# Kernel tuning notes

Measured on AMD Instinct MI355X. Metric: run time of the kernel, lower is better.

The kernel has to match this reference:

```python
import jax, jax.numpy as jnp
import numpy as np

N_NODES = 100000
N_EDGES = 1600000
IN_DIM = 128
HID = 128
OUT_DIM = 64
N_LAYERS = 3


def setup_inputs() -> dict:
    key = jax.random.key(0)
    ks = jax.random.split(key, 8)
    x = jax.random.normal(ks[0], (N_NODES, IN_DIM), dtype=jnp.float32)
    edge_index = jax.random.randint(ks[1], (2, N_EDGES), 0, N_NODES, dtype=jnp.int64)
    s = 1.0 / np.sqrt(HID)
    Wl = jax.random.normal(ks[2], (N_LAYERS, HID, HID), dtype=jnp.float32) * s
    Wr = jax.random.normal(ks[3], (N_LAYERS, HID, HID), dtype=jnp.float32) * s
    b = jnp.zeros((N_LAYERS, HID), dtype=jnp.float32)
    fc_w = jax.random.normal(ks[4], (N_LAYERS * HID, OUT_DIM), dtype=jnp.float32) * (1.0 / np.sqrt(N_LAYERS * HID))
    fc_b = jnp.zeros((OUT_DIM,), dtype=jnp.float32)
    return {"x": x, "edge_index": edge_index, "Wl": Wl, "Wr": Wr, "b": b, "fc_w": fc_w, "fc_b": fc_b}


def _sage_conv(x, src, dst, Wl, Wr, b, n_nodes):
    # PyG SAGEConv (aggr='mean'): out = lin_l(mean_{j->i} x_j) + lin_r(x_i)
    msg = x[src]                                             # [E, d] gather
    agg = jax.ops.segment_sum(msg, dst, num_segments=n_nodes)  # [N, d]
    deg = jax.ops.segment_sum(jnp.ones((src.shape[0],), x.dtype), dst, num_segments=n_nodes)
    mean = agg / jnp.maximum(deg, 1.0)[:, None]
    return mean @ Wl + x @ Wr + b


def reference(x, edge_index, Wl, Wr, b, fc_w, fc_b):
    src, dst = edge_index[0], edge_index[1]
    n = x.shape[0]
    h = x
    layer_out = []
    for i in range(N_LAYERS):  # small fixed layer count
        h = jax.nn.relu(_sage_conv(h, src, dst, Wl[i], Wr[i], b[i], n))
        layer_out.append(h)  # dropout p=0 -> identity
    hk = jnp.concatenate(layer_out, axis=-1)  # JK 'cat': [N, L*HID]
    return hk @ fc_w + fc_b
```

## Files before the change

kernel.cpp:

```cpp
#include <hip/hip_runtime.h>
#include <hip/hip_bf16.h>
#include <stdint.h>

#define N_NODES 100000
#define N_EDGES 1600000
#define HID 128
#define OUT_DIM 64
#define N_LAYERS 3
#define CAP 64
#define CAP_SHIFT 6
#define BIN_NODES 256
#define NBIN2 ((N_NODES + BIN_NODES - 1) / BIN_NODES)
#define BINCAP 8192
#define EPT 8
#define P1_BLOCKS ((N_EDGES + 256 * EPT - 1) / (256 * EPT))

typedef __attribute__((ext_vector_type(8))) short short8;
typedef __attribute__((ext_vector_type(4))) float v4f;
typedef __attribute__((ext_vector_type(4))) unsigned short ushort4v;

__device__ __forceinline__ float bf2f(unsigned int lo16) {
    union { unsigned int i; float f; } v; v.i = lo16 << 16; return v.f;
}
__device__ __forceinline__ unsigned short f2bf(float f) {
    union { float f; unsigned int i; } v; v.f = f;
    unsigned int r = v.i + 0x7fffu + ((v.i >> 16) & 1u);
    return (unsigned short)(r >> 16);
}

__device__ __forceinline__ void stage16(const void* g, void* l) {
    __builtin_amdgcn_global_load_lds(
        (const __attribute__((address_space(1))) unsigned int*)g,
        (__attribute__((address_space(3))) unsigned int*)l, 16, 0, 0);
}

#define CONV_N (N_NODES * HID / 4)
__global__ __launch_bounds__(256) void merged_pre(
    const int* __restrict__ raw,
    int* __restrict__ bin_cnt, unsigned int* __restrict__ bins,
    const float* __restrict__ x, unsigned short* __restrict__ xb,
    const float* __restrict__ Wl, const float* __restrict__ Wr,
    const float* __restrict__ fc_w,
    unsigned short* __restrict__ WlT, unsigned short* __restrict__ WrT,
    unsigned short* __restrict__ fcT,
    unsigned short* b0, unsigned short* b1, unsigned short* b2) {
    __shared__ int h[NBIN2];
    __shared__ int basekeep[NBIN2];
    __shared__ int sflag;
    int blk = blockIdx.x, tid = threadIdx.x;

    if (blk < P1_BLOCKS) {
        if (tid < 64) {
            int v = raw[2 * tid + 1];
            unsigned long long bl = __ballot(v != 0);
            if (tid == 0) sflag = (bl == 0ull) ? 1 : 0;
        }
        for (int b = tid; b < NBIN2; b += 256) h[b] = 0;
        __syncthreads();
        bool is64 = (sflag != 0);

        int e0 = blk * (256 * EPT) + tid;
        int s[EPT], d[EPT];
#pragma unroll
        for (int k = 0; k < EPT; ++k) {
            int e = e0 + k * 256;
            if (e < N_EDGES) {
                if (is64) {
                    const long long* r = (const long long*)raw;
                    d[k] = (int)r[N_EDGES + e];
                    s[k] = (int)r[e];
                } else {
                    d[k] = raw[N_EDGES + e];
                    s[k] = raw[e];
                }
            } else {
                d[k] = -1;
            }
        }
#pragma unroll
        for (int k = 0; k < EPT; ++k)
            if (d[k] >= 0) atomicAdd(&h[d[k] >> 8], 1);
        __syncthreads();
        for (int b = tid; b < NBIN2; b += 256) {
            int c = h[b];
            basekeep[b] = c ? atomicAdd(&bin_cnt[b], c) : 0;
            h[b] = 0;
        }
        __syncthreads();
#pragma unroll
        for (int k = 0; k < EPT; ++k) {
            if (d[k] >= 0) {
                int b = d[k] >> 8;
                int off = basekeep[b] + atomicAdd(&h[b], 1);
                if (off < BINCAP)
                    bins[(size_t)b * BINCAP + off] =
                        ((unsigned int)s[k] << 8) | (unsigned int)(d[k] & 255);
            }
        }
    }

    if (blk == P1_BLOCKS && tid < 192) {
        unsigned short* bufs[3] = {b0, b1, b2};
        uint32_t* p = (uint32_t*)bufs[tid >> 6];
        p[(size_t)N_NODES * 64 + (tid & 63)] = 0;
    }

    int gidx = blk * 256 + tid;
    if (gidx < CONV_N) {
        float4 v = ((const float4*)x)[gidx];
        ushort4v o;
        o[0] = f2bf(v.x); o[1] = f2bf(v.y); o[2] = f2bf(v.z); o[3] = f2bf(v.w);
        ((ushort4v*)xb)[gidx] = o;
    } else {
        int idx = gidx - CONV_N;
        const int WELEMS = N_LAYERS * HID * HID;
        if (idx < WELEMS) {
            int l = idx / (HID * HID);
            int rem = idx - l * HID * HID;
            int k = rem / HID, nn2 = rem - k * HID;
            WlT[l * HID * HID + nn2 * HID + k] = f2bf(Wl[idx]);
            WrT[l * HID * HID + nn2 * HID + k] = f2bf(Wr[idx]);
        } else {
            int j = idx - WELEMS;
            if (j < N_LAYERS * HID * OUT_DIM) {
                int l = j / (HID * OUT_DIM);
                int rem = j - l * HID * OUT_DIM;
                int k = rem / OUT_DIM, o = rem - k * OUT_DIM;
                fcT[l * OUT_DIM * HID + o * HID + k] = f2bf(fc_w[(l * HID + k) * OUT_DIM + o]);
            }
        }
    }
}

__global__ __launch_bounds__(256) void fill_p2(const int* __restrict__ bin_cnt,
                                               const unsigned int* __restrict__ bins,
                                               int* __restrict__ ell,
                                               int* __restrict__ deg,
                                               float* __restrict__ inv_deg, int n) {
    __shared__ int tile[BIN_NODES * CAP];
    __shared__ int cnt[BIN_NODES];
    int b = blockIdx.x, tid = threadIdx.x;
    for (int i = tid; i < BIN_NODES; i += 256) cnt[i] = 0;
    __syncthreads();

    int m = bin_cnt[b];
    if (m > BINCAP) m = BINCAP;
    for (int i = tid; i < m; i += 256) {
        unsigned int e = bins[(size_t)b * BINCAP + i];
        int dl = (int)(e & 255u);
        int slot = atomicAdd(&cnt[dl], 1);
        if (slot < CAP) tile[(dl << CAP_SHIFT) + slot] = (int)(e >> 8);
    }
    __syncthreads();

    int node0 = b << 8;
    for (int i = tid; i < BIN_NODES; i += 256) {
        int node = node0 + i;
        if (node < n) {
            int dgf = cnt[i];
            int dg = dgf > CAP ? CAP : dgf;
            deg[node] = dg;
            inv_deg[node] = 1.0f / (float)(dg > 0 ? dg : 1);
            int r = (dg + 7) & ~7;
            for (int p = dg; p < r; ++p) tile[(i << CAP_SHIFT) + p] = N_NODES;
        }
    }
    __syncthreads();

    const uint4* t4 = (const uint4*)tile;
    uint4* g4 = (uint4*)ell;
    for (int v = tid; v < BIN_NODES * 16; v += 256) {
        int row = v >> 4;
        int node = node0 + row;
        if (node < n) g4[((size_t)node << 4) + (v & 15)] = t4[v];
    }
}

__device__ __forceinline__ void gather8(const uint4* __restrict__ hv,
                                        int4 i0, int4 i1, int lane16, uint4 v[8]) {
    v[0] = hv[(size_t)i0.x * 16 + lane16];
    v[1] = hv[(size_t)i0.y * 16 + lane16];
    v[2] = hv[(size_t)i0.z * 16 + lane16];
    v[3] = hv[(size_t)i0.w * 16 + lane16];
    v[4] = hv[(size_t)i1.x * 16 + lane16];
    v[5] = hv[(size_t)i1.y * 16 + lane16];
    v[6] = hv[(size_t)i1.z * 16 + lane16];
    v[7] = hv[(size_t)i1.w * 16 + lane16];
}
__device__ __forceinline__ void accum8(const uint4 v[8], float a[8]) {
#pragma unroll
    for (int u = 0; u < 8; ++u) {
        a[0] += bf2f(v[u].x & 0xffffu); a[1] += bf2f(v[u].x >> 16);
        a[2] += bf2f(v[u].y & 0xffffu); a[3] += bf2f(v[u].y >> 16);
        a[4] += bf2f(v[u].z & 0xffffu); a[5] += bf2f(v[u].z >> 16);
        a[6] += bf2f(v[u].w & 0xffffu); a[7] += bf2f(v[u].w >> 16);
    }
}

__global__ __launch_bounds__(256) void agg_bf(
    const unsigned short* __restrict__ h, const int* __restrict__ ell,
    const int* __restrict__ deg, const float* __restrict__ inv_deg,
    unsigned short* __restrict__ meanb) {
    int tid = threadIdx.x;
    int grp = tid >> 4;
    int lane16 = tid & 15;
    int node = blockIdx.x * 16 + grp;
    bool valid = node < N_NODES;
    int nd = valid ? node : 0;
    int dg = valid ? deg[nd] : 0;
    int dgp = (dg + 7) & ~7;
    int base = nd << CAP_SHIFT;
    const uint4* hv = (const uint4*)h;
    float a[8];
#pragma unroll
    for (int c = 0; c < 8; ++c) a[c] = 0.f;

    if (dgp) {
        uint4 vA[8], vB[8];
        int4 i0 = *(const int4*)&ell[base + 0];
        int4 i1 = *(const int4*)&ell[base + 4];
        gather8(hv, i0, i1, lane16, vA);
        int t = 8;
        bool done = false;
        while (t < dgp) {
            i0 = *(const int4*)&ell[base + t];
            i1 = *(const int4*)&ell[base + t + 4];
            gather8(hv, i0, i1, lane16, vB);
            accum8(vA, a);
            t += 8;
            if (t >= dgp) { accum8(vB, a); done = true; break; }
            i0 = *(const int4*)&ell[base + t];
            i1 = *(const int4*)&ell[base + t + 4];
            gather8(hv, i0, i1, lane16, vA);
            accum8(vB, a);
            t += 8;
        }
        if (!done) accum8(vA, a);
    }
    if (valid) {
        float id = inv_deg[nd];
        uint4 o;
        o.x = (uint32_t)f2bf(a[0] * id) | ((uint32_t)f2bf(a[1] * id) << 16);
        o.y = (uint32_t)f2bf(a[2] * id) | ((uint32_t)f2bf(a[3] * id) << 16);
        o.z = (uint32_t)f2bf(a[4] * id) | ((uint32_t)f2bf(a[5] * id) << 16);
        o.w = (uint32_t)f2bf(a[6] * id) | ((uint32_t)f2bf(a[7] * id) << 16);
        *(uint4*)&meanb[(size_t)node * HID + lane16 * 8] = o;
    }
}

__global__ __launch_bounds__(256, 2) void layer_mfma(
    const unsigned short* __restrict__ Am,
    const unsigned short* __restrict__ Ah,
    const unsigned short* __restrict__ WlT,
    const unsigned short* __restrict__ WrT,
    const float* __restrict__ bias,
    unsigned short* __restrict__ Hout, int n) {
    __shared__ uint4 smA[128 * 16];
    __shared__ uint4 smB[128 * 16];
    int tid = threadIdx.x;
    int w = tid >> 6, L = tid & 63;
    int q = L >> 4, r16 = L & 15;
    int colbase = (w & 1) * 64;
    int nodebase = (w >> 1) * 64;
    int node0 = blockIdx.x * 128;

    {
        const unsigned short* srcs[2] = {Am, Ah};
#pragma unroll
        for (int op = 0; op < 2; ++op) {
            const unsigned short* S = srcs[op];
            char* D = (char*)(op ? smB : smA);
#pragma unroll
            for (int i = 0; i < 8; ++i) {
                int c = (w << 3) + i;
                int row_l = (c << 2) + (L >> 4);
                int chunk = (L & 15) ^ (row_l & 7);
                const unsigned short* src =
                    S + (((size_t)(node0 + row_l)) << 7) + (chunk << 3);
                stage16(src, D + (c << 10));
            }
        }
    }

    short8 wfr[2][4][4];
#pragma unroll
    for (int seg = 0; seg < 2; ++seg) {
        const unsigned short* WT = seg ? WrT : WlT;
#pragma unroll
        for (int t = 0; t < 4; ++t)
#pragma unroll
            for (int i = 0; i < 4; ++i)
                wfr[seg][t][i] =
                    *(const short8*)&WT[(colbase + i * 16 + r16) * HID + t * 32 + q * 8];
    }

    __syncthreads();

    v4f acc[4][4];
#pragma unroll
    for (int i = 0; i < 4; ++i)
#pragma unroll
        for (int j = 0; j < 4; ++j)
#pragma unroll
            for (int r = 0; r < 4; ++r) acc[i][j][r] = 0.f;

#pragma unroll
    for (int seg = 0; seg < 2; ++seg) {
        const uint4* SM = seg ? smB : smA;
#pragma unroll
        for (int t = 0; t < 4; ++t) {
            short8 bfr[4];
#pragma unroll
            for (int j = 0; j < 4; ++j) {
                int row = nodebase + j * 16 + r16;
                bfr[j] = *(const short8*)&SM[(row << 4) + ((t * 4 + q) ^ (row & 7))];
            }
#pragma unroll
            for (int i = 0; i < 4; ++i)
#pragma unroll
                for (int j = 0; j < 4; ++j)
                    acc[i][j] = __builtin_amdgcn_mfma_f32_16x16x32_bf16(
                        wfr[seg][t][i], bfr[j], acc[i][j], 0, 0, 0);
        }
    }

#pragma unroll
    for (int i = 0; i < 4; ++i) {
        int col = colbase + i * 16 + q * 4;
        float4 bv = *(const float4*)&bias[col];
#pragma unroll
        for (int j = 0; j < 4; ++j) {
            int node = node0 + nodebase + j * 16 + r16;
            if (node < n) {
                float v0 = acc[i][j][0] + bv.x;
                float v1 = acc[i][j][1] + bv.y;
                float v2 = acc[i][j][2] + bv.z;
                float v3 = acc[i][j][3] + bv.w;
                ushort4v o;
                o[0] = f2bf(v0 > 0.f ? v0 : 0.f);
                o[1] = f2bf(v1 > 0.f ? v1 : 0.f);
                o[2] = f2bf(v2 > 0.f ? v2 : 0.f);
                o[3] = f2bf(v3 > 0.f ? v3 : 0.f);
                *(ushort4v*)&Hout[(size_t)node * HID + col] = o;
            }
        }
    }
}

__global__ __launch_bounds__(256, 2) void layer3_fc(
    const unsigned short* __restrict__ Am,
    const unsigned short* __restrict__ Ah,
    const unsigned short* __restrict__ WlT,
    const unsigned short* __restrict__ WrT,
    const float* __restrict__ bias,
    const unsigned short* __restrict__ hA,
    const unsigned short* __restrict__ fcT,
    const float* __restrict__ fc_b,
    float* __restrict__ out, int n) {
    __shared__ uint4 smA[128 * 16];
    __shared__ uint4 smB[128 * 16];
    int tid = threadIdx.x;
    int w = tid >> 6, L = tid & 63;
    int q = L >> 4, r16 = L & 15;
    int colbase = (w & 1) * 64;
    int nodebase = (w >> 1) * 64;
    int node0 = blockIdx.x * 128;

    {
        const unsigned short* srcs[2] = {Am, Ah};
#pragma unroll
        for (int op = 0; op < 2; ++op) {
            const unsigned short* S = srcs[op];
            char* D = (char*)(op ? smB : smA);
#pragma unroll
            for (int i = 0; i < 8; ++i) {
                int c = (w << 3) + i;
                int row_l = (c << 2) + (L >> 4);
                int chunk = (L & 15) ^ (row_l & 7);
                const unsigned short* src =
                    S + (((size_t)(node0 + row_l)) << 7) + (chunk << 3);
                stage16(src, D + (c << 10));
            }
        }
    }

    short8 wfr[2][4][4];
#pragma unroll
    for (int seg = 0; seg < 2; ++seg) {
        const unsigned short* WT = seg ? WrT : WlT;
#pragma unroll
        for (int t = 0; t < 4; ++t)
#pragma unroll
            for (int i = 0; i < 4; ++i)
                wfr[seg][t][i] =
                    *(const short8*)&WT[(colbase + i * 16 + r16) * HID + t * 32 + q * 8];
    }

    __syncthreads();

    v4f acc[4][4];
#pragma unroll
    for (int i = 0; i < 4; ++i)
#pragma unroll
        for (int j = 0; j < 4; ++j)
#pragma unroll
            for (int r = 0; r < 4; ++r) acc[i][j][r] = 0.f;

#pragma unroll
    for (int seg = 0; seg < 2; ++seg) {
        const uint4* SM = seg ? smB : smA;
#pragma unroll
        for (int t = 0; t < 4; ++t) {
            short8 bfr[4];
#pragma unroll
            for (int j = 0; j < 4; ++j) {
                int row = nodebase + j * 16 + r16;
                bfr[j] = *(const short8*)&SM[(row << 4) + ((t * 4 + q) ^ (row & 7))];
            }
#pragma unroll
            for (int i = 0; i < 4; ++i)
#pragma unroll
                for (int j = 0; j < 4; ++j)
                    acc[i][j] = __builtin_amdgcn_mfma_f32_16x16x32_bf16(
                        wfr[seg][t][i], bfr[j], acc[i][j], 0, 0, 0);
        }
    }

    int nd2[2], gvalid[2];
#pragma unroll
    for (int j = 0; j < 2; ++j) {
        int t = node0 + w * 32 + j * 16 + r16;
        gvalid[j] = t < n;
        nd2[j] = gvalid[j] ? t : n - 1;
    }
    short8 ha[2][4];
#pragma unroll
    for (int j = 0; j < 2; ++j)
#pragma unroll
        for (int t = 0; t < 4; ++t)
            ha[j][t] = *(const short8*)&hA[(size_t)nd2[j] * HID + t * 32 + q * 8];

    __syncthreads();

#pragma unroll
    for (int i = 0; i < 4; ++i) {
        int col = colbase + i * 16 + q * 4;
        float4 bv = *(const float4*)&bias[col];
#pragma unroll
        for (int j = 0; j < 4; ++j) {
            int row = nodebase + j * 16 + r16;
            float v0 = acc[i][j][0] + bv.x;
            float v1 = acc[i][j][1] + bv.y;
            float v2 = acc[i][j][2] + bv.z;
            float v3 = acc[i][j][3] + bv.w;
            uint2 val;
            val.x = (uint32_t)f2bf(v0 > 0.f ? v0 : 0.f) |
                    ((uint32_t)f2bf(v1 > 0.f ? v1 : 0.f) << 16);
            val.y = (uint32_t)f2bf(v2 > 0.f ? v2 : 0.f) |
                    ((uint32_t)f2bf(v3 > 0.f ? v3 : 0.f) << 16);
            int slot = (col >> 3) ^ (row & 7);
            uint2* p2 = (uint2*)&smA[(row << 4) + slot];
            p2[q & 1] = val;
        }
    }
    __syncthreads();

    v4f acc2[4][2];
#pragma unroll
    for (int i = 0; i < 4; ++i) {
        float4 bv = *(const float4*)&fc_b[i * 16 + q * 4];
#pragma unroll
        for (int j = 0; j < 2; ++j) {
            acc2[i][j][0] = bv.x; acc2[i][j][1] = bv.y;
            acc2[i][j][2] = bv.z; acc2[i][j][3] = bv.w;
        }
    }

#pragma unroll
    for (int l = 0; l < 3; ++l) {
        const unsigned short* F = fcT + (size_t)l * OUT_DIM * HID;
#pragma unroll
        for (int t = 0; t < 4; ++t) {
            int koff = t * 32 + q * 8;
            short8 afr[4], bfr[2];
#pragma unroll
            for (int i = 0; i < 4; ++i)
                afr[i] = *(const short8*)&F[(i * 16 + r16) * HID + koff];
#pragma unroll
            for (int j = 0; j < 2; ++j) {
                int row = w * 32 + j * 16 + r16;
                if (l == 0)
                    bfr[j] = ha[j][t];
                else if (l == 1)
                    bfr[j] = *(const short8*)&smB[(row << 4) + ((t * 4 + q) ^ (row & 7))];
                else
                    bfr[j] = *(const short8*)&smA[(row << 4) + ((t * 4 + q) ^ (row & 7))];
            }
#pragma unroll
            for (int i = 0; i < 4; ++i)
#pragma unroll
                for (int j = 0; j < 2; ++j)
                    acc2[i][j] = __builtin_amdgcn_mfma_f32_16x16x32_bf16(afr[i], bfr[j], acc2[i][j], 0, 0, 0);
        }
    }

#pragma unroll
    for (int i = 0; i < 4; ++i)
#pragma unroll
        for (int j = 0; j < 2; ++j)
            if (gvalid[j])
                *(v4f*)&out[(size_t)nd2[j] * OUT_DIM + i * 16 + q * 4] = acc2[i][j];
}

extern "C" void kernel_launch(void* const* d_in, const int* in_sizes, int n_in,
                              void* d_out, int out_size, void* d_ws, size_t ws_size,
                              hipStream_t stream) {
    const float* x     = (const float*)d_in[0];
    const int*   edges = (const int*)d_in[1];
    const float* Wl    = (const float*)d_in[2];
    const float* Wr    = (const float*)d_in[3];
    const float* b     = (const float*)d_in[4];
    const float* fc_w  = (const float*)d_in[5];
    const float* fc_b  = (const float*)d_in[6];
    float* out = (float*)d_out;

    char* ws = (char*)d_ws;
    size_t off = 0;
    auto alloc = [&](size_t bytes) {
        void* p = ws + off;
        off = (off + bytes + 255) & ~(size_t)255;
        return p;
    };
    int*   bin_cnt = (int*)alloc((size_t)NBIN2 * 4);
    int*   deg     = (int*)alloc((size_t)N_NODES * 4);
    float* inv_deg = (float*)alloc((size_t)N_NODES * 4);
    int*   ell     = (int*)alloc(((size_t)N_NODES * CAP + 64) * 4);
    unsigned int* bins = (unsigned int*)alloc((size_t)NBIN2 * BINCAP * 4);
    unsigned short* xb    = (unsigned short*)alloc((size_t)(N_NODES + 128) * HID * 2);
    unsigned short* meanb = (unsigned short*)alloc((size_t)(N_NODES + 128) * HID * 2);
    unsigned short* hA    = (unsigned short*)alloc((size_t)(N_NODES + 128) * HID * 2);
    unsigned short* hB    = (unsigned short*)alloc((size_t)(N_NODES + 128) * HID * 2);
    unsigned short* WlT   = (unsigned short*)alloc((size_t)N_LAYERS * HID * HID * 2);
    unsigned short* WrT   = (unsigned short*)alloc((size_t)N_LAYERS * HID * HID * 2);
    unsigned short* fcT   = (unsigned short*)alloc((size_t)N_LAYERS * OUT_DIM * HID * 2);

    hipMemsetAsync(bin_cnt, 0, (size_t)NBIN2 * 4, stream);

    const int PREP_TOTAL = CONV_N + N_LAYERS * HID * HID + N_LAYERS * HID * OUT_DIM;
    int pregrid = (PREP_TOTAL + 255) / 256;
    merged_pre<<<pregrid, 256, 0, stream>>>(
        edges, bin_cnt, bins, x, xb, Wl, Wr, fc_w, WlT, WrT, fcT, xb, hA, hB);
    fill_p2<<<NBIN2, 256, 0, stream>>>(bin_cnt, bins, ell, deg, inv_deg, N_NODES);

    int ngrid = (N_NODES + 127) / 128;
    int agrid = (N_NODES + 15) / 16;

    agg_bf<<<agrid, 256, 0, stream>>>(xb, ell, deg, inv_deg, meanb);
    layer_mfma<<<ngrid, 256, 0, stream>>>(
        meanb, xb, WlT, WrT, b, hA, N_NODES);

    agg_bf<<<agrid, 256, 0, stream>>>(hA, ell, deg, inv_deg, meanb);
    layer_mfma<<<ngrid, 256, 0, stream>>>(
        meanb, hA, WlT + (size_t)HID * HID, WrT + (size_t)HID * HID, b + HID, hB, N_NODES);

    agg_bf<<<agrid, 256, 0, stream>>>(hB, ell, deg, inv_deg, meanb);
    layer3_fc<<<ngrid, 256, 0, stream>>>(
        meanb, hB, WlT + (size_t)2 * HID * HID, WrT + (size_t)2 * HID * HID, b + 2 * HID,
        hA, fcT, fc_b, out, N_NODES);
}
```

Before: 446.6 us.

## Simplify aggregation loop and shrink layer GEMM tile to 64 nodes for occupancy

The aggregation kernel drops its manual double-buffered gather pipeline for a simple per-8-neighbor loop with scalar index loads, leaving latency hiding to the compiler and occupancy. The layer GEMM kernel now handles 64 nodes per block, with each wave owning 32 output columns, which halves shared memory and accumulator registers and raises the launch-bounds occupancy hint from 2 to 4. The cost is less in-flight memory parallelism per thread in aggregation and more blocks, with weight fragments reloaded for each smaller tile.

```diff
diff --git a/kernel.cpp b/kernel.cpp
--- a/kernel.cpp
+++ b/kernel.cpp
@@ -176,27 +176,6 @@
     }
 }
 
-__device__ __forceinline__ void gather8(const uint4* __restrict__ hv,
-                                        int4 i0, int4 i1, int lane16, uint4 v[8]) {
-    v[0] = hv[(size_t)i0.x * 16 + lane16];
-    v[1] = hv[(size_t)i0.y * 16 + lane16];
-    v[2] = hv[(size_t)i0.z * 16 + lane16];
-    v[3] = hv[(size_t)i0.w * 16 + lane16];
-    v[4] = hv[(size_t)i1.x * 16 + lane16];
-    v[5] = hv[(size_t)i1.y * 16 + lane16];
-    v[6] = hv[(size_t)i1.z * 16 + lane16];
-    v[7] = hv[(size_t)i1.w * 16 + lane16];
-}
-__device__ __forceinline__ void accum8(const uint4 v[8], float a[8]) {
-#pragma unroll
-    for (int u = 0; u < 8; ++u) {
-        a[0] += bf2f(v[u].x & 0xffffu); a[1] += bf2f(v[u].x >> 16);
-        a[2] += bf2f(v[u].y & 0xffffu); a[3] += bf2f(v[u].y >> 16);
-        a[4] += bf2f(v[u].z & 0xffffu); a[5] += bf2f(v[u].z >> 16);
-        a[6] += bf2f(v[u].w & 0xffffu); a[7] += bf2f(v[u].w >> 16);
-    }
-}
-
 __global__ __launch_bounds__(256) void agg_bf(
     const unsigned short* __restrict__ h, const int* __restrict__ ell,
     const int* __restrict__ deg, const float* __restrict__ inv_deg,
@@ -215,27 +194,20 @@
 #pragma unroll
     for (int c = 0; c < 8; ++c) a[c] = 0.f;
 
-    if (dgp) {
-        uint4 vA[8], vB[8];
-        int4 i0 = *(const int4*)&ell[base + 0];
-        int4 i1 = *(const int4*)&ell[base + 4];
-        gather8(hv, i0, i1, lane16, vA);
-        int t = 8;
-        bool done = false;
-        while (t < dgp) {
-            i0 = *(const int4*)&ell[base + t];
-            i1 = *(const int4*)&ell[base + t + 4];
-            gather8(hv, i0, i1, lane16, vB);
-            accum8(vA, a);
-            t += 8;
-            if (t >= dgp) { accum8(vB, a); done = true; break; }
-            i0 = *(const int4*)&ell[base + t];
-            i1 = *(const int4*)&ell[base + t + 4];
-            gather8(hv, i0, i1, lane16, vA);
-            accum8(vB, a);
-            t += 8;
-        }
-        if (!done) accum8(vA, a);
+    for (int t = 0; t < dgp; t += 8) {
+        int idx[8];
+#pragma unroll
+        for (int u = 0; u < 8; ++u) idx[u] = ell[base + t + u];
+        uint4 v[8];
+#pragma unroll
+        for (int u = 0; u < 8; ++u) v[u] = hv[(size_t)idx[u] * 16 + lane16];
+#pragma unroll
+        for (int u = 0; u < 8; ++u) {
+            a[0] += bf2f(v[u].x & 0xffffu); a[1] += bf2f(v[u].x >> 16);
+            a[2] += bf2f(v[u].y & 0xffffu); a[3] += bf2f(v[u].y >> 16);
+            a[4] += bf2f(v[u].z & 0xffffu); a[5] += bf2f(v[u].z >> 16);
+            a[6] += bf2f(v[u].w & 0xffffu); a[7] += bf2f(v[u].w >> 16);
+        }
     }
     if (valid) {
         float id = inv_deg[nd];
@@ -248,21 +220,20 @@
     }
 }
 
-__global__ __launch_bounds__(256, 2) void layer_mfma(
+__global__ __launch_bounds__(256, 4) void layer_mfma(
     const unsigned short* __restrict__ Am,
     const unsigned short* __restrict__ Ah,
     const unsigned short* __restrict__ WlT,
     const unsigned short* __restrict__ WrT,
     const float* __restrict__ bias,
     unsigned short* __restrict__ Hout, int n) {
-    __shared__ uint4 smA[128 * 16];
-    __shared__ uint4 smB[128 * 16];
+    __shared__ uint4 smA[64 * 16];
+    __shared__ uint4 smB[64 * 16];
     int tid = threadIdx.x;
     int w = tid >> 6, L = tid & 63;
     int q = L >> 4, r16 = L & 15;
-    int colbase = (w & 1) * 64;
-    int nodebase = (w >> 1) * 64;
-    int node0 = blockIdx.x * 128;
+    int colbase = w << 5;
+    int node0 = blockIdx.x * 64;
 
     {
         const unsigned short* srcs[2] = {Am, Ah};
@@ -271,8 +242,8 @@
             const unsigned short* S = srcs[op];
             char* D = (char*)(op ? smB : smA);
 #pragma unroll
-            for (int i = 0; i < 8; ++i) {
-                int c = (w << 3) + i;
+            for (int i = 0; i < 4; ++i) {
+                int c = (w << 2) + i;
                 int row_l = (c << 2) + (L >> 4);
                 int chunk = (L & 15) ^ (row_l & 7);
                 const unsigned short* src =
@@ -282,23 +253,23 @@
         }
     }
 
-    short8 wfr[2][4][4];
+    short8 wfr[2][4][2];
 #pragma unroll
     for (int seg = 0; seg < 2; ++seg) {
         const unsigned short* WT = seg ? WrT : WlT;
 #pragma unroll
         for (int t = 0; t < 4; ++t)
 #pragma unroll
-            for (int i = 0; i < 4; ++i)
+            for (int i = 0; i < 2; ++i)
                 wfr[seg][t][i] =
                     *(const short8*)&WT[(colbase + i * 16 + r16) * HID + t * 32 + q * 8];
     }
 
     __syncthreads();
 
-    v4f acc[4][4];
-#pragma unroll
-    for (int i = 0; i < 4; ++i)
+    v4f acc[2][4];
+#pragma unroll
+    for (int i = 0; i < 2; ++i)
 #pragma unroll
         for (int j = 0; j < 4; ++j)
 #pragma unroll
@@ -312,11 +283,11 @@
             short8 bfr[4];
 #pragma unroll
             for (int j = 0; j < 4; ++j) {
-                int row = nodebase + j * 16 + r16;
+                int row = j * 16 + r16;
                 bfr[j] = *(const short8*)&SM[(row << 4) + ((t * 4 + q) ^ (row & 7))];
             }
 #pragma unroll
-            for (int i = 0; i < 4; ++i)
+            for (int i = 0; i < 2; ++i)
 #pragma unroll
                 for (int j = 0; j < 4; ++j)
                     acc[i][j] = __builtin_amdgcn_mfma_f32_16x16x32_bf16(
@@ -325,12 +296,12 @@
     }
 
 #pragma unroll
-    for (int i = 0; i < 4; ++i) {
+    for (int i = 0; i < 2; ++i) {
         int col = colbase + i * 16 + q * 4;
         float4 bv = *(const float4*)&bias[col];
 #pragma unroll
         for (int j = 0; j < 4; ++j) {
-            int node = node0 + nodebase + j * 16 + r16;
+            int node = node0 + j * 16 + r16;
             if (node < n) {
                 float v0 = acc[i][j][0] + bv.x;
                 float v1 = acc[i][j][1] + bv.y;
@@ -552,19 +523,20 @@
         edges, bin_cnt, bins, x, xb, Wl, Wr, fc_w, WlT, WrT, fcT, xb, hA, hB);
     fill_p2<<<NBIN2, 256, 0, stream>>>(bin_cnt, bins, ell, deg, inv_deg, N_NODES);
 
-    int ngrid = (N_NODES + 127) / 128;
+    int lgrid = (N_NODES + 63) / 64;
+    int fgrid = (N_NODES + 127) / 128;
     int agrid = (N_NODES + 15) / 16;
 
     agg_bf<<<agrid, 256, 0, stream>>>(xb, ell, deg, inv_deg, meanb);
-    layer_mfma<<<ngrid, 256, 0, stream>>>(
+    layer_mfma<<<lgrid, 256, 0, stream>>>(
         meanb, xb, WlT, WrT, b, hA, N_NODES);
 
     agg_bf<<<agrid, 256, 0, stream>>>(hA, ell, deg, inv_deg, meanb);
-    layer_mfma<<<ngrid, 256, 0, stream>>>(
+    layer_mfma<<<lgrid, 256, 0, stream>>>(
         meanb, hA, WlT + (size_t)HID * HID, WrT + (size_t)HID * HID, b + HID, hB, N_NODES);
 
     agg_bf<<<agrid, 256, 0, stream>>>(hB, ell, deg, inv_deg, meanb);
-    layer3_fc<<<ngrid, 256, 0, stream>>>(
+    layer3_fc<<<fgrid, 256, 0, stream>>>(
         meanb, hB, WlT + (size_t)2 * HID * HID, WrT + (size_t)2 * HID * HID, b + 2 * HID,
         hA, fcT, fc_b, out, N_NODES);
 }
```

Result: faster. 425.8 us, median of 2 (-4.7%).
